# Kernel tuning notes

Measured on AMD Instinct MI355X. Metric: run time of the kernel, lower is better.

The kernel has to match this reference:

```python
import jax, jax.numpy as jnp
import numpy as np

N = 100000
E = 1600000
NFEAT = 128
NHID1 = 128
NHID2 = 128
NCLASS = 40


def setup_inputs() -> dict:
    key = jax.random.key(0)
    ks = jax.random.split(key, 16)
    x = jax.random.normal(ks[0], (N, NFEAT), dtype=jnp.float32)
    src = jax.random.randint(ks[1], (E,), 0, N, dtype=jnp.int32)
    dst = jax.random.randint(ks[2], (E,), 0, N, dtype=jnp.int32)
    s = 0.05
    params = {
        # SAGE layer 1: self branch and neighbor branch
        'w1s': jax.random.normal(ks[3], (NFEAT, NHID1), dtype=jnp.float32) * s,
        'b1s': jnp.zeros((NHID1,), dtype=jnp.float32),
        'w1n': jax.random.normal(ks[4], (NFEAT, NHID1), dtype=jnp.float32) * s,
        'b1n': jnp.zeros((NHID1,), dtype=jnp.float32),
        # SAGE layer 2 (input dim 2*NHID1)
        'w2s': jax.random.normal(ks[5], (2 * NHID1, NHID2), dtype=jnp.float32) * s,
        'b2s': jnp.zeros((NHID2,), dtype=jnp.float32),
        'w2n': jax.random.normal(ks[6], (2 * NHID1, NHID2), dtype=jnp.float32) * s,
        'b2n': jnp.zeros((NHID2,), dtype=jnp.float32),
        # final linear head (input dim 2*NHID2)
        'wfc': jax.random.normal(ks[7], (2 * NHID2, NCLASS), dtype=jnp.float32) * s,
        'bfc': jnp.zeros((NCLASS,), dtype=jnp.float32),
    }
    return {'x': x, 'src': src, 'dst': dst, **params}


def _neigh_mean(h, src, dst, n_nodes):
    # mean aggregation == spmm(row-normalized adj, h), via segment sum over edges
    msg = jax.ops.segment_sum(h[src], dst, num_segments=n_nodes)  # [N, d]
    cnt = jax.ops.segment_sum(jnp.ones((src.shape[0],), h.dtype), dst, num_segments=n_nodes)
    return msg / jnp.maximum(cnt, 1.0)[:, None]


def _sage_layer(h, src, dst, ws, bs, wn, bn):
    neigh = _neigh_mean(h, src, dst, h.shape[0])
    return jnp.concatenate([h @ ws + bs, neigh @ wn + bn], axis=1)


def _l2_normalize(h, eps=1e-12):
    nrm = jnp.sqrt(jnp.sum(h * h, axis=1, keepdims=True))
    return h / jnp.maximum(nrm, eps)


def reference(x, src, dst, w1s, b1s, w1n, b1n, w2s, b2s, w2n, b2n, wfc, bfc):
    h = jax.nn.relu(_sage_layer(x, src, dst, w1s, b1s, w1n, b1n))  # [N, 2*NHID1]
    h = _l2_normalize(h)
    # dropout is identity in eval mode
    h = jax.nn.relu(_sage_layer(h, src, dst, w2s, b2s, w2n, b2n))  # [N, 2*NHID2]
    h = _l2_normalize(h)
    return h @ wfc + bfc  # [N, NCLASS]
```

## Files before the change

kernel.cpp:

```cpp
#include <hip/hip_runtime.h>
#include <hip/hip_bf16.h>


#define N_NODES 100000
#define N_EDGES 1600000
#define NBUCK   196
#define BCAP    12288
#define PB_CAP  14336
#define CHUNK   4096
#define PREP_BLKS 432
#define GEMM1_BLKS 782

typedef unsigned short u16;
typedef unsigned int u32;
typedef __bf16 bf16x8 __attribute__((ext_vector_type(8)));
typedef float  f32x4  __attribute__((ext_vector_type(4)));

__device__ __forceinline__ u16 f2b(float f) {
  unsigned x = __builtin_bit_cast(unsigned, f);
  unsigned r = x + 0x7fffu + ((x >> 16) & 1u);
  return (u16)(r >> 16);
}
__device__ __forceinline__ bf16x8 ldfrag(const u16* p) {
  uint4 u = *reinterpret_cast<const uint4*>(p);
  return __builtin_bit_cast(bf16x8, u);
}
__device__ __forceinline__ void unpack8(uint4 u, float* f) {
  f[0] = __builtin_bit_cast(float, u.x << 16);
  f[1] = __builtin_bit_cast(float, u.x & 0xffff0000u);
  f[2] = __builtin_bit_cast(float, u.y << 16);
  f[3] = __builtin_bit_cast(float, u.y & 0xffff0000u);
  f[4] = __builtin_bit_cast(float, u.z << 16);
  f[5] = __builtin_bit_cast(float, u.z & 0xffff0000u);
  f[6] = __builtin_bit_cast(float, u.w << 16);
  f[7] = __builtin_bit_cast(float, u.w & 0xffff0000u);
}
__device__ __forceinline__ uint4 pack8(const float* f) {
  uint4 u;
  u.x = (u32)f2b(f[0]) | ((u32)f2b(f[1]) << 16);
  u.y = (u32)f2b(f[2]) | ((u32)f2b(f[3]) << 16);
  u.z = (u32)f2b(f[4]) | ((u32)f2b(f[5]) << 16);
  u.w = (u32)f2b(f[6]) | ((u32)f2b(f[7]) << 16);
  return u;
}

__device__ __forceinline__ int wave_incl_scan(int x, int lane) {
#pragma unroll
  for (int d = 1; d < 64; d <<= 1) {
    int n = __shfl_up(x, d, 64);
    if (lane >= d) x += n;
  }
  return x;
}

__device__ void prep_body(int bid, const float* __restrict__ w1s,
                          const float* __restrict__ w1n,
                          const float* __restrict__ w2s,
                          const float* __restrict__ w2n,
                          const float* __restrict__ wfc, u16* __restrict__ WT1,
                          u16* __restrict__ WT2, u16* __restrict__ WFCT) {
  int i = bid * 256 + threadIdx.x;
  if (i < 32768) {
    int c = i >> 7, k = i & 127;
    float v = (c < 128) ? w1s[k * 128 + c] : w1n[k * 128 + (c - 128)];
    WT1[c * 128 + k] = f2b(v);
  } else if (i < 32768 + 65536) {
    int j = i - 32768;
    int c = j >> 8, k = j & 255;
    float v = (c < 128) ? w2s[k * 128 + c] : w2n[k * 128 + (c - 128)];
    WT2[c * 256 + k] = f2b(v);
  } else {
    int j = i - 98304;
    int c = j >> 8, k = j & 255;
    float v = (c < 40) ? wfc[k * 40 + c] : 0.f;
    WFCT[c * 256 + k] = f2b(v);
  }
}

__global__ __launch_bounds__(256) void prep_bucket_kernel(
    const float* __restrict__ w1s, const float* __restrict__ w1n,
    const float* __restrict__ w2s, const float* __restrict__ w2n,
    const float* __restrict__ wfc, u16* __restrict__ WT1,
    u16* __restrict__ WT2, u16* __restrict__ WFCT,
    const int* __restrict__ src, const int* __restrict__ dst,
    int* __restrict__ cntg, u32* __restrict__ pairBuf) {
  if (blockIdx.x < PREP_BLKS) {
    prep_body(blockIdx.x, w1s, w1n, w2s, w2n, wfc, WT1, WT2, WFCT);
    return;
  }
  __shared__ unsigned hist[NBUCK];
  __shared__ unsigned gbase[NBUCK];
  __shared__ int sws[4];
  __shared__ u32 stage[CHUNK];
  __shared__ int tgt[CHUNK];
  const int tid = threadIdx.x, lane = tid & 63, wid = tid >> 6;
  const int e0 = (blockIdx.x - PREP_BLKS) * CHUNK;

  for (int i = tid; i < NBUCK; i += 256) hist[i] = 0u;
  __syncthreads();

  u32 myW[16];
  int myR[16], myB[16];
#pragma unroll
  for (int k = 0; k < 16; ++k) {
    int e = e0 + k * 256 + tid;
    if (e < N_EDGES) {
      unsigned d = (unsigned)dst[e];
      myW[k] = ((d & 511u) << 17) | (unsigned)src[e];
      myB[k] = (int)(d >> 9);
      myR[k] = (int)atomicAdd(&hist[myB[k]], 1u);
    } else {
      myB[k] = -1;
    }
  }
  __syncthreads();

  int cnt = (tid < NBUCK) ? (int)hist[tid] : 0;
  int inc = wave_incl_scan(cnt, lane);
  if (lane == 63) sws[wid] = inc;
  __syncthreads();
  if (wid == 0) {
    int s = (lane < 4) ? sws[lane] : 0;
    s = wave_incl_scan(s, lane);
    if (lane < 4) sws[lane] = s;
  }
  __syncthreads();
  int excl = (wid ? sws[wid - 1] : 0) + inc - cnt;
  int gofs = 0;
  if (tid < NBUCK && cnt > 0) gofs = tid * BCAP + atomicAdd(&cntg[tid], cnt);
  __syncthreads();
  if (tid < NBUCK) {
    hist[tid] = (unsigned)excl;
    gbase[tid] = (unsigned)gofs;
  }
  __syncthreads();

#pragma unroll
  for (int k = 0; k < 16; ++k) {
    if (myB[k] >= 0) {
      int slot = (int)hist[myB[k]] + myR[k];
      stage[slot] = myW[k];
      tgt[slot] = (int)gbase[myB[k]] + myR[k];
    }
  }
  __syncthreads();
  int nvalid = N_EDGES - e0;
  if (nvalid > CHUNK) nvalid = CHUNK;
  for (int i = tid; i < nvalid; i += 256) pairBuf[tgt[i]] = stage[i];
}

__device__ void csr_body(char* smem, int b, const u32* __restrict__ pairBuf,
                         const int* __restrict__ cntg, int* __restrict__ rowptr,
                         int* __restrict__ degA, int* __restrict__ csr) {
  int* lcnt = (int*)smem;
  int* lofs = lcnt + 512;
  int* sws = lofs + 512;
  int* cstage = sws + 8;
  const int tid = threadIdx.x;
  const int lane = tid & 63, wid = tid >> 6;
  int nb = cntg[b];
  if (nb > BCAP) nb = BCAP;
  const u32* pp = pairBuf + (size_t)b * BCAP;

  lcnt[tid] = 0;
  __syncthreads();
  for (int i = tid; i < nb; i += 512) atomicAdd(&lcnt[(pp[i] >> 17) & 511], 1);
  __syncthreads();
  int dg = lcnt[tid];
  int pd = (dg + 7) & ~7;
  int inc = wave_incl_scan(pd, lane);
  if (lane == 63) sws[wid] = inc;
  __syncthreads();
  if (wid == 0) {
    int s = (lane < 8) ? sws[lane] : 0;
    s = wave_incl_scan(s, lane);
    if (lane < 8) sws[lane] = s;
  }
  __syncthreads();
  int excl = (wid ? sws[wid - 1] : 0) + inc - pd;
  int ptot = sws[7];
  int node = b * 512 + tid;
  if (node < N_NODES) {
    rowptr[node] = b * PB_CAP + excl;
    degA[node] = dg;
  }
  lofs[tid] = excl;
  __syncthreads();
  for (int i = tid; i < nb; i += 512) {
    u32 pr = pp[i];
    int pos = atomicAdd(&lofs[(pr >> 17) & 511], 1);
    if (pos < PB_CAP) cstage[pos] = (int)(pr & 0x1FFFFu);
  }
  __syncthreads();
  for (int k = excl + dg; k < excl + pd; ++k)
    if (k < PB_CAP) cstage[k] = N_NODES;
  __syncthreads();
  if (ptot > PB_CAP) ptot = PB_CAP;
  for (int i = tid; i < ptot; i += 512) csr[b * PB_CAP + i] = cstage[i];
}

__device__ void gemm1_body(char* smem, int bid, const float* __restrict__ A,
                           const u16* __restrict__ WT, u16* __restrict__ Cs,
                           u16* __restrict__ Cn) {
  u16* lb = (u16*)smem;
  char* lbc = smem;
  const int tid = threadIdx.x;
  for (int i = tid; i < 4096; i += 512) {
    uint4 v = *reinterpret_cast<const uint4*>(WT + i * 8);
    int byte = i * 16;
    int swz = byte ^ (((byte >> 8) & 7) << 4);
    *reinterpret_cast<uint4*>(lbc + swz) = v;
  }

  const int w = tid >> 6, lane = tid & 63;
  const int lrow = lane & 15, lk = lane >> 4;
  const int xr = (lrow & 7) << 4;
  const int rbase = bid * 128 + w * 16;

  bf16x8 af[4];
  {
    int r = rbase + lrow;
    if (r >= N_NODES) r = N_NODES - 1;
    const float* ap = A + (size_t)r * 128 + lk * 8;
#pragma unroll
    for (int ks = 0; ks < 4; ++ks) {
      float4 f0 = *reinterpret_cast<const float4*>(ap + ks * 32);
      float4 f1 = *reinterpret_cast<const float4*>(ap + ks * 32 + 4);
      float f[8] = {f0.x, f0.y, f0.z, f0.w, f1.x, f1.y, f1.z, f1.w};
      af[ks] = __builtin_bit_cast(bf16x8, pack8(f));
    }
  }
  __syncthreads();

  f32x4 acc[16];
#pragma unroll
  for (int ct = 0; ct < 16; ++ct) acc[ct] = f32x4{0.f, 0.f, 0.f, 0.f};
#pragma unroll
  for (int ks = 0; ks < 4; ++ks) {
#pragma unroll
    for (int ct = 0; ct < 16; ++ct) {
      int byte = (ct * 16 + lrow) * 256 + ks * 64 + lk * 16;
      bf16x8 b = __builtin_bit_cast(
          bf16x8, *reinterpret_cast<const uint4*>(lbc + (byte ^ xr)));
      acc[ct] = __builtin_amdgcn_mfma_f32_16x16x32_bf16(af[ks], b, acc[ct], 0, 0, 0);
    }
  }
#pragma unroll
  for (int j = 0; j < 4; ++j) {
    int r = rbase + lk * 4 + j;
    if (r < N_NODES) {
      u16* cs = Cs + (size_t)r * 128 + lrow;
      u16* cn = Cn + (size_t)r * 128 + lrow;
#pragma unroll
      for (int ct = 0; ct < 8; ++ct) cs[ct * 16] = f2b(acc[ct][j]);
#pragma unroll
      for (int ct = 0; ct < 8; ++ct) cn[ct * 16] = f2b(acc[8 + ct][j]);
    }
  }
}

__global__ __launch_bounds__(512) void csr_gemm1_kernel(
    const u32* __restrict__ pairBuf, const int* __restrict__ cntg,
    int* __restrict__ rowptr, int* __restrict__ degA, int* __restrict__ csr,
    const float* __restrict__ A, const u16* __restrict__ WT,
    u16* __restrict__ Cs, u16* __restrict__ Cn) {
  extern __shared__ char smem[];
  if (blockIdx.x < NBUCK) {
    csr_body(smem, blockIdx.x, pairBuf, cntg, rowptr, degA, csr);
  } else {
    gemm1_body(smem, blockIdx.x - NBUCK, A, WT, Cs, Cn);
  }
}

__device__ __forceinline__ void agg_node(
    const u16* __restrict__ Xs, const u16* __restrict__ Xn,
    const int* __restrict__ rowptr, const int* __restrict__ degA,
    const int* __restrict__ csr, const float* __restrict__ bs,
    const float* __restrict__ bn, int node, int g, int lc,
    float* sf, float* nf) {
  int beg = rowptr[node], dg = degA[node];
  int cnt = (dg + 7) & ~7;
  float acc[8] = {0.f, 0.f, 0.f, 0.f, 0.f, 0.f, 0.f, 0.f};
  const u16* colbase = Xn + lc * 8;
  const int* cp = csr + beg;
  for (int j = 0; j < cnt; j += 8) {
    int s0 = cp[j + g];
    int s1 = cp[j + 4 + g];
    uint4 u0 = *reinterpret_cast<const uint4*>(colbase + (size_t)s0 * 128);
    uint4 u1 = *reinterpret_cast<const uint4*>(colbase + (size_t)s1 * 128);
    float f0[8], f1[8];
    unpack8(u0, f0);
    unpack8(u1, f1);
#pragma unroll
    for (int i = 0; i < 8; ++i) acc[i] += f0[i] + f1[i];
  }
#pragma unroll
  for (int i = 0; i < 8; ++i) {
    acc[i] += __shfl_xor(acc[i], 32, 64);
    acc[i] += __shfl_xor(acc[i], 16, 64);
  }
  float inv = 1.f / (float)(dg > 0 ? dg : 1);
  uint4 sv4 = *reinterpret_cast<const uint4*>(Xs + (size_t)node * 128 + lc * 8);
  unpack8(sv4, sf);
  float4 b0 = *reinterpret_cast<const float4*>(bs + lc * 8);
  float4 b1 = *reinterpret_cast<const float4*>(bs + lc * 8 + 4);
  float4 c0 = *reinterpret_cast<const float4*>(bn + lc * 8);
  float4 c1 = *reinterpret_cast<const float4*>(bn + lc * 8 + 4);
  float bsv[8] = {b0.x, b0.y, b0.z, b0.w, b1.x, b1.y, b1.z, b1.w};
  float bnv[8] = {c0.x, c0.y, c0.z, c0.w, c1.x, c1.y, c1.z, c1.w};
  float ss = 0.f;
#pragma unroll
  for (int i = 0; i < 8; ++i) {
    sf[i] = fmaxf(sf[i] + bsv[i], 0.f);
    nf[i] = fmaxf(acc[i] * inv + bnv[i], 0.f);
    ss += sf[i] * sf[i] + nf[i] * nf[i];
  }
  ss += __shfl_xor(ss, 1, 64);
  ss += __shfl_xor(ss, 2, 64);
  ss += __shfl_xor(ss, 4, 64);
  ss += __shfl_xor(ss, 8, 64);
  float sc = 1.f / fmaxf(sqrtf(ss), 1e-12f);
#pragma unroll
  for (int i = 0; i < 8; ++i) {
    sf[i] *= sc;
    nf[i] *= sc;
  }
}

__global__ __launch_bounds__(256) void agg_epi_kernel(
    const u16* __restrict__ Xs, const u16* __restrict__ Xn,
    const int* __restrict__ rowptr, const int* __restrict__ degA,
    const int* __restrict__ csr, const float* __restrict__ bs,
    const float* __restrict__ bn, u16* __restrict__ H) {
  const int lane = threadIdx.x & 63;
  const int g = lane >> 4, lc = lane & 15;
  const int wave0 = blockIdx.x * 4 + (threadIdx.x >> 6);
  const int stride = gridDim.x * 4;
  for (int node = wave0; node < N_NODES; node += stride) {
    float sf[8], nf[8];
    agg_node(Xs, Xn, rowptr, degA, csr, bs, bn, node, g, lc, sf, nf);
    if (g == 0) {
      *reinterpret_cast<uint4*>(H + (size_t)node * 256 + lc * 8) = pack8(sf);
    } else if (g == 1) {
      *reinterpret_cast<uint4*>(H + (size_t)node * 256 + 128 + lc * 8) = pack8(nf);
    }
  }
}

__global__ __launch_bounds__(512) void gemm2_kernel(
    const u16* __restrict__ A, const u16* __restrict__ WT,
    u16* __restrict__ Cs, u16* __restrict__ Cn) {
  __shared__ u16 lb[128 * 256];
  char* lbc = reinterpret_cast<char*>(lb);
  const int tid = threadIdx.x;
  const int w = tid >> 6, lane = tid & 63;
  const int lrow = lane & 15, lk = lane >> 4;
  const int xr = (lrow & 7) << 4;
  const int rbase = blockIdx.x * 128 + w * 16;

  bf16x8 af[8];
  {
    int r = rbase + lrow;
    if (r >= N_NODES) r = N_NODES - 1;
    const u16* ap = A + (size_t)r * 256 + lk * 8;
#pragma unroll
    for (int ks = 0; ks < 8; ++ks) af[ks] = ldfrag(ap + ks * 32);
  }

#pragma unroll
  for (int half = 0; half < 2; ++half) {
    const u16* Wsrc = WT + (size_t)half * 128 * 256;
    for (int i = tid; i < 4096; i += 512) {
      uint4 v = *reinterpret_cast<const uint4*>(Wsrc + i * 8);
      int byte = i * 16;
      int swz = byte ^ (((byte >> 9) & 7) << 4);
      *reinterpret_cast<uint4*>(lbc + swz) = v;
    }
    __syncthreads();

    f32x4 acc[8];
#pragma unroll
    for (int ct = 0; ct < 8; ++ct) acc[ct] = f32x4{0.f, 0.f, 0.f, 0.f};
#pragma unroll
    for (int ks = 0; ks < 8; ++ks) {
#pragma unroll
      for (int ct = 0; ct < 8; ++ct) {
        int byte = (ct * 16 + lrow) * 512 + ks * 64 + lk * 16;
        bf16x8 b = __builtin_bit_cast(
            bf16x8, *reinterpret_cast<const uint4*>(lbc + (byte ^ xr)));
        acc[ct] = __builtin_amdgcn_mfma_f32_16x16x32_bf16(af[ks], b, acc[ct], 0, 0, 0);
      }
    }
    u16* __restrict__ Cout = half ? Cn : Cs;
#pragma unroll
    for (int j = 0; j < 4; ++j) {
      int r = rbase + lk * 4 + j;
      if (r < N_NODES) {
        u16* cp = Cout + (size_t)r * 128 + lrow;
#pragma unroll
        for (int ct = 0; ct < 8; ++ct) cp[ct * 16] = f2b(acc[ct][j]);
      }
    }
    __syncthreads();
  }
}

__global__ __launch_bounds__(512) void agg_fc_kernel(
    const u16* __restrict__ Xs, const u16* __restrict__ Xn,
    const int* __restrict__ rowptr, const int* __restrict__ degA,
    const int* __restrict__ csr, const float* __restrict__ bs,
    const float* __restrict__ bn, const u16* __restrict__ WFCT,
    const float* __restrict__ bfc, float* __restrict__ Out) {
  __shared__ u16 hh[32 * 256];
  char* hhb = reinterpret_cast<char*>(hh);
  const int tid = threadIdx.x, w = tid >> 6, lane = tid & 63;
  const int g = lane >> 4, lc = lane & 15;
  const int nb0 = blockIdx.x * 32;

  for (int t = 0; t < 4; ++t) {
    int r = w * 4 + t;
    int node = nb0 + r;
    int xr_r = (r & 7) << 4;
    uint4 val;
    int cbyte;
    if (node < N_NODES) {
      float sf[8], nf[8];
      agg_node(Xs, Xn, rowptr, degA, csr, bs, bn, node, g, lc, sf, nf);
      val = (g == 0) ? pack8(sf) : pack8(nf);
    } else {
      val = uint4{0u, 0u, 0u, 0u};
    }
    if (g == 0) {
      cbyte = (lc * 16) ^ xr_r;
      *reinterpret_cast<uint4*>(hhb + r * 512 + cbyte) = val;
    } else if (g == 1) {
      cbyte = 256 + ((lc * 16) ^ xr_r);
      *reinterpret_cast<uint4*>(hhb + r * 512 + cbyte) = val;
    }
  }
  __syncthreads();

  const int rt = w & 1, cg = w >> 1;
  if (cg < 3) {
    const int lrow = lane & 15, lk = lane >> 4;
    const int arow = rt * 16 + lrow;
    const int xr_a = (arow & 7) << 4;
    f32x4 acc = {0.f, 0.f, 0.f, 0.f};
#pragma unroll
    for (int ks = 0; ks < 8; ++ks) {
      int cbyte = (ks * 64 + lk * 16) ^ xr_a;
      bf16x8 a = __builtin_bit_cast(
          bf16x8, *reinterpret_cast<const uint4*>(hhb + arow * 512 + cbyte));
      bf16x8 b = ldfrag(WFCT + (size_t)(cg * 16 + lrow) * 256 + ks * 32 + lk * 8);
      acc = __builtin_amdgcn_mfma_f32_16x16x32_bf16(a, b, acc, 0, 0, 0);
    }
#pragma unroll
    for (int j = 0; j < 4; ++j) {
      int row = nb0 + rt * 16 + lk * 4 + j;
      int col = cg * 16 + lrow;
      if (row < N_NODES && col < 40) Out[(size_t)row * 40 + col] = acc[j] + bfc[col];
    }
  }
}

extern "C" void kernel_launch(void* const* d_in, const int* in_sizes, int n_in,
                              void* d_out, int out_size, void* d_ws, size_t ws_size,
                              hipStream_t stream) {
  const float* x = (const float*)d_in[0];
  const int* src = (const int*)d_in[1];
  const int* dst = (const int*)d_in[2];
  const float* w1s = (const float*)d_in[3];
  const float* b1s = (const float*)d_in[4];
  const float* w1n = (const float*)d_in[5];
  const float* b1n = (const float*)d_in[6];
  const float* w2s = (const float*)d_in[7];
  const float* b2s = (const float*)d_in[8];
  const float* w2n = (const float*)d_in[9];
  const float* b2n = (const float*)d_in[10];
  const float* wfc = (const float*)d_in[11];
  const float* bfc = (const float*)d_in[12];
  float* out = (float*)d_out;

  char* p = (char*)d_ws;
  auto alloc = [&](size_t bytes) {
    char* r = p;
    p += (bytes + 255) & ~(size_t)255;
    return r;
  };
  u16* XWs = (u16*)alloc((size_t)N_NODES * 128 * 2);
  u16* XWn = (u16*)alloc(((size_t)N_NODES + 1) * 128 * 2);
  u16* h1 = (u16*)alloc((size_t)N_NODES * 256 * 2);
  u16* WT1 = (u16*)alloc(32768 * 2);
  u16* WT2 = (u16*)alloc(65536 * 2);
  u16* WFCT = (u16*)alloc(12288 * 2);
  u32* pairBuf = (u32*)alloc((size_t)NBUCK * BCAP * 4);
  int* cntg = (int*)alloc(NBUCK * 4);
  int* rowptr = (int*)alloc((size_t)N_NODES * 4);
  int* degA = (int*)alloc((size_t)N_NODES * 4);
  int* csr = (int*)alloc((size_t)NBUCK * PB_CAP * 4);

  hipMemsetAsync(cntg, 0, NBUCK * 4, stream);
  hipMemsetAsync(XWn + (size_t)N_NODES * 128, 0, 256, stream);

  prep_bucket_kernel<<<PREP_BLKS + 391, 256, 0, stream>>>(
      w1s, w1n, w2s, w2n, wfc, WT1, WT2, WFCT, src, dst, cntg, pairBuf);
  csr_gemm1_kernel<<<NBUCK + GEMM1_BLKS, 512, 65536, stream>>>(
      pairBuf, cntg, rowptr, degA, csr, x, WT1, XWs, XWn);
  agg_epi_kernel<<<2048, 256, 0, stream>>>(XWs, XWn, rowptr, degA, csr, b1s, b1n, h1);
  gemm2_kernel<<<GEMM1_BLKS, 512, 0, stream>>>(h1, WT2, XWs, XWn);
  agg_fc_kernel<<<3125, 512, 0, stream>>>(XWs, XWn, rowptr, degA, csr, b2s, b2n,
                                          WFCT, bfc, out);
}
```

Measured before the change: 360.9 us.

## Unfuse layer-2 aggregation from FC head and unroll gather to 16 edges

The fused agg_fc kernel is replaced by a second launch of the layer-1 aggregation epilogue kernel, which writes h2 to a buffer, followed by a separate FC GEMM kernel that stages the FC weights in LDS. This removes the MFMA phase that left some waves idle and the sync inside the gather kernel, at the cost of an extra global write and read of the 256-wide bf16 hidden state. Separately, the gather loop processes 16 edges per iteration instead of 8 to expose more memory-level parallelism. This requires CSR rows padded to 16, which adds more dummy-node loads for low-degree nodes.

```diff
diff --git a/kernel.cpp b/kernel.cpp
--- a/kernel.cpp
+++ b/kernel.cpp
@@ -167,7 +167,7 @@
   for (int i = tid; i < nb; i += 512) atomicAdd(&lcnt[(pp[i] >> 17) & 511], 1);
   __syncthreads();
   int dg = lcnt[tid];
-  int pd = (dg + 7) & ~7;
+  int pd = (dg + 15) & ~15;
   int inc = wave_incl_scan(pd, lane);
   if (lane == 63) sws[wid] = inc;
   __syncthreads();
@@ -202,7 +202,6 @@
 __device__ void gemm1_body(char* smem, int bid, const float* __restrict__ A,
                            const u16* __restrict__ WT, u16* __restrict__ Cs,
                            u16* __restrict__ Cn) {
-  u16* lb = (u16*)smem;
   char* lbc = smem;
   const int tid = threadIdx.x;
   for (int i = tid; i < 4096; i += 512) {
@@ -279,20 +278,26 @@
     const float* __restrict__ bn, int node, int g, int lc,
     float* sf, float* nf) {
   int beg = rowptr[node], dg = degA[node];
-  int cnt = (dg + 7) & ~7;
+  int cnt = (dg + 15) & ~15;
   float acc[8] = {0.f, 0.f, 0.f, 0.f, 0.f, 0.f, 0.f, 0.f};
   const u16* colbase = Xn + lc * 8;
   const int* cp = csr + beg;
-  for (int j = 0; j < cnt; j += 8) {
+  for (int j = 0; j < cnt; j += 16) {
     int s0 = cp[j + g];
     int s1 = cp[j + 4 + g];
+    int s2 = cp[j + 8 + g];
+    int s3 = cp[j + 12 + g];
     uint4 u0 = *reinterpret_cast<const uint4*>(colbase + (size_t)s0 * 128);
     uint4 u1 = *reinterpret_cast<const uint4*>(colbase + (size_t)s1 * 128);
-    float f0[8], f1[8];
+    uint4 u2 = *reinterpret_cast<const uint4*>(colbase + (size_t)s2 * 128);
+    uint4 u3 = *reinterpret_cast<const uint4*>(colbase + (size_t)s3 * 128);
+    float f0[8], f1[8], f2[8], f3[8];
     unpack8(u0, f0);
     unpack8(u1, f1);
-#pragma unroll
-    for (int i = 0; i < 8; ++i) acc[i] += f0[i] + f1[i];
+    unpack8(u2, f2);
+    unpack8(u3, f3);
+#pragma unroll
+    for (int i = 0; i < 8; ++i) acc[i] += (f0[i] + f1[i]) + (f2[i] + f3[i]);
   }
 #pragma unroll
   for (int i = 0; i < 8; ++i) {
@@ -405,60 +410,56 @@
   }
 }
 
-__global__ __launch_bounds__(512) void agg_fc_kernel(
-    const u16* __restrict__ Xs, const u16* __restrict__ Xn,
-    const int* __restrict__ rowptr, const int* __restrict__ degA,
-    const int* __restrict__ csr, const float* __restrict__ bs,
-    const float* __restrict__ bn, const u16* __restrict__ WFCT,
-    const float* __restrict__ bfc, float* __restrict__ Out) {
-  __shared__ u16 hh[32 * 256];
-  char* hhb = reinterpret_cast<char*>(hh);
-  const int tid = threadIdx.x, w = tid >> 6, lane = tid & 63;
-  const int g = lane >> 4, lc = lane & 15;
-  const int nb0 = blockIdx.x * 32;
-
-  for (int t = 0; t < 4; ++t) {
-    int r = w * 4 + t;
-    int node = nb0 + r;
-    int xr_r = (r & 7) << 4;
-    uint4 val;
-    int cbyte;
-    if (node < N_NODES) {
-      float sf[8], nf[8];
-      agg_node(Xs, Xn, rowptr, degA, csr, bs, bn, node, g, lc, sf, nf);
-      val = (g == 0) ? pack8(sf) : pack8(nf);
-    } else {
-      val = uint4{0u, 0u, 0u, 0u};
-    }
-    if (g == 0) {
-      cbyte = (lc * 16) ^ xr_r;
-      *reinterpret_cast<uint4*>(hhb + r * 512 + cbyte) = val;
-    } else if (g == 1) {
-      cbyte = 256 + ((lc * 16) ^ xr_r);
-      *reinterpret_cast<uint4*>(hhb + r * 512 + cbyte) = val;
-    }
-  }
-  __syncthreads();
-
-  const int rt = w & 1, cg = w >> 1;
-  if (cg < 3) {
-    const int lrow = lane & 15, lk = lane >> 4;
-    const int arow = rt * 16 + lrow;
-    const int xr_a = (arow & 7) << 4;
-    f32x4 acc = {0.f, 0.f, 0.f, 0.f};
-#pragma unroll
-    for (int ks = 0; ks < 8; ++ks) {
-      int cbyte = (ks * 64 + lk * 16) ^ xr_a;
-      bf16x8 a = __builtin_bit_cast(
-          bf16x8, *reinterpret_cast<const uint4*>(hhb + arow * 512 + cbyte));
-      bf16x8 b = ldfrag(WFCT + (size_t)(cg * 16 + lrow) * 256 + ks * 32 + lk * 8);
-      acc = __builtin_amdgcn_mfma_f32_16x16x32_bf16(a, b, acc, 0, 0, 0);
-    }
-#pragma unroll
-    for (int j = 0; j < 4; ++j) {
-      int row = nb0 + rt * 16 + lk * 4 + j;
-      int col = cg * 16 + lrow;
-      if (row < N_NODES && col < 40) Out[(size_t)row * 40 + col] = acc[j] + bfc[col];
+__global__ __launch_bounds__(256) void fc_kernel(const u16* __restrict__ H2,
+                                                 const u16* __restrict__ WFCT,
+                                                 const float* __restrict__ bfc,
+                                                 float* __restrict__ Out) {
+  __shared__ u16 lb[48 * 256];
+  char* lbc = reinterpret_cast<char*>(lb);
+  const int tid = threadIdx.x;
+#pragma unroll
+  for (int i = tid; i < 48 * 256 / 8; i += 256) {
+    uint4 v = *reinterpret_cast<const uint4*>(WFCT + i * 8);
+    int byte = i * 16;
+    int swz = byte ^ (((byte >> 9) & 7) << 4);
+    *reinterpret_cast<uint4*>(lbc + swz) = v;
+  }
+  __syncthreads();
+  const int w = tid >> 6, lane = tid & 63;
+  const int lrow = lane & 15, lk = lane >> 4;
+  const int xr = (lrow & 7) << 4;
+  const int rbase = blockIdx.x * 64 + w * 16;
+
+  bf16x8 af[8];
+  {
+    int r = rbase + lrow;
+    if (r >= N_NODES) r = N_NODES - 1;
+    const u16* ap = H2 + (size_t)r * 256 + lk * 8;
+#pragma unroll
+    for (int ks = 0; ks < 8; ++ks) af[ks] = ldfrag(ap + ks * 32);
+  }
+  f32x4 acc[3];
+#pragma unroll
+  for (int ct = 0; ct < 3; ++ct) acc[ct] = f32x4{0.f, 0.f, 0.f, 0.f};
+#pragma unroll
+  for (int ks = 0; ks < 8; ++ks) {
+#pragma unroll
+    for (int ct = 0; ct < 3; ++ct) {
+      int byte = (ct * 16 + lrow) * 512 + ks * 64 + lk * 16;
+      bf16x8 b = __builtin_bit_cast(
+          bf16x8, *reinterpret_cast<const uint4*>(lbc + (byte ^ xr)));
+      acc[ct] = __builtin_amdgcn_mfma_f32_16x16x32_bf16(af[ks], b, acc[ct], 0, 0, 0);
+    }
+  }
+#pragma unroll
+  for (int j = 0; j < 4; ++j) {
+    int r = rbase + lk * 4 + j;
+    if (r < N_NODES) {
+#pragma unroll
+      for (int ct = 0; ct < 3; ++ct) {
+        int col = ct * 16 + lrow;
+        if (col < 40) Out[(size_t)r * 40 + col] = acc[ct][j] + bfc[col];
+      }
     }
   }
 }
@@ -498,6 +499,7 @@
   int* rowptr = (int*)alloc((size_t)N_NODES * 4);
   int* degA = (int*)alloc((size_t)N_NODES * 4);
   int* csr = (int*)alloc((size_t)NBUCK * PB_CAP * 4);
+  u16* h2 = h1;
 
   hipMemsetAsync(cntg, 0, NBUCK * 4, stream);
   hipMemsetAsync(XWn + (size_t)N_NODES * 128, 0, 256, stream);
@@ -508,6 +510,6 @@
       pairBuf, cntg, rowptr, degA, csr, x, WT1, XWs, XWn);
   agg_epi_kernel<<<2048, 256, 0, stream>>>(XWs, XWn, rowptr, degA, csr, b1s, b1n, h1);
   gemm2_kernel<<<GEMM1_BLKS, 512, 0, stream>>>(h1, WT2, XWs, XWn);
-  agg_fc_kernel<<<3125, 512, 0, stream>>>(XWs, XWn, rowptr, degA, csr, b2s, b2n,
-                                          WFCT, bfc, out);
-}
+  agg_epi_kernel<<<2048, 256, 0, stream>>>(XWs, XWn, rowptr, degA, csr, b2s, b2n, h2);
+  fc_kernel<<<1563, 256, 0, stream>>>(h2, WFCT, bfc, out);
+}
```

New measurement: 372.8 us. 3.3% more time.
